# Optimization experiments

Hardware: AMD Instinct MI355X
Metric: run time of the kernel (lower is better)

## Reference

```python
import jax, jax.numpy as jnp
import numpy as np


def setup_inputs() -> dict:
    key = jax.random.key(0)
    k1, k2, k3 = jax.random.split(key, 3)
    worker_num, task_num, edge_type, ability_num = 2048, 2048, 16, 64
    # inputs stacks worker feature rows [:worker_num, :ability_num]
    # and task label-probability rows [worker_num:, :edge_type]
    inputs = jax.random.uniform(k1, (worker_num + task_num, ability_num), dtype=jnp.float32)
    W = jax.random.normal(k2, (ability_num, 1), dtype=jnp.float32)
    b = jax.random.normal(k3, (1,), dtype=jnp.float32)
    return {
        "inputs": inputs,
        "W": W,
        "b": b,
        "worker_num": worker_num,
        "task_num": task_num,
        "edge_type": edge_type,
        "ability_num": ability_num,
    }


def reference(inputs, W, b, worker_num, task_num, edge_type, ability_num):
    # Worker features: [Wn, A]; task label distributions tau: [T, L]
    worker_feature = inputs[:worker_num, :ability_num]
    tau = inputs[worker_num:, :edge_type]
    # prob_part1 = sigmoid(w_i . W + b): per-worker correctness probability, [Wn, 1]
    p1 = jax.nn.sigmoid(worker_feature @ W + b)
    # prob_part2: remaining mass spread over the other (L-1) labels, [Wn, 1]
    p2 = (1.0 - p1) / jnp.float32(edge_type - 1)
    # P[i,j,l] = p1[i]^tau[j,l] * p2[i]^(1 - tau[j,l])  -> [Wn, T, L]
    p1 = p1[:, :, None]  # [Wn, 1, 1]
    p2 = p2[:, :, None]
    tau_b = tau[None, :, :]  # [1, T, L]
    P = jnp.power(p1, tau_b) * jnp.power(p2, 1.0 - tau_b)
    return P
```

## Files before the change

kernel.cpp:

```cpp
#include <hip/hip_runtime.h>

#define WORKERS 2048
#define TASKS   2048
#define ETYPE   16
#define ABIL    64

#define PER_WORKER (TASKS * ETYPE)
#define PER_WORKER4 (PER_WORKER / 4)
#define TOTAL4 (WORKERS * TASKS * ETYPE / 4)

__global__ void prep_kernel(const float* __restrict__ inputs,
                            const float* __restrict__ W,
                            const float* __restrict__ b,
                            float* __restrict__ l1,
                            float* __restrict__ l2,
                            float* __restrict__ tauc) {
    const int tid = blockIdx.x * blockDim.x + threadIdx.x;

    if (tid < WORKERS) {
        const float4* row = reinterpret_cast<const float4*>(inputs + (size_t)tid * ABIL);
        const float4* Wv  = reinterpret_cast<const float4*>(W);
        float acc = 0.0f;
#pragma unroll
        for (int k = 0; k < ABIL / 4; ++k) {
            float4 x = row[k];
            float4 w = Wv[k];
            acc = fmaf(x.x, w.x, acc);
            acc = fmaf(x.y, w.y, acc);
            acc = fmaf(x.z, w.z, acc);
            acc = fmaf(x.w, w.w, acc);
        }
        acc += b[0];
        const float LOG2E = 1.4426950408889634f;
        float e = __builtin_amdgcn_exp2f(-acc * LOG2E);
        float p1 = 1.0f / (1.0f + e);
        float p2 = (1.0f - p1) * (1.0f / (ETYPE - 1));
        l1[tid] = __builtin_amdgcn_logf(p1);
        l2[tid] = __builtin_amdgcn_logf(p2);
    }

    if (tid < PER_WORKER4) {
        int t  = tid >> 2;
        int e0 = (tid & 3) * 4;
        const float4* src = reinterpret_cast<const float4*>(
            inputs + (size_t)(WORKERS + t) * ABIL + e0);
        reinterpret_cast<float4*>(tauc)[tid] = *src;
    }
}

__global__ void __launch_bounds__(256)
pow_kernel(const float* __restrict__ l1,
           const float* __restrict__ l2,
           const float* __restrict__ tauc,
           float4* __restrict__ out) {
    const int stride = gridDim.x * blockDim.x;
    for (int i = blockIdx.x * blockDim.x + threadIdx.x; i < TOTAL4; i += stride) {
        const int w    = i >> 13;
        const int rem4 = i & (PER_WORKER4 - 1);
        const float4 tau = reinterpret_cast<const float4*>(tauc)[rem4];
        const float a = l1[w];
        const float c = l2[w];
        float4 r;
        r.x = __builtin_amdgcn_exp2f(fmaf(tau.x, a, (1.0f - tau.x) * c));
        r.y = __builtin_amdgcn_exp2f(fmaf(tau.y, a, (1.0f - tau.y) * c));
        r.z = __builtin_amdgcn_exp2f(fmaf(tau.z, a, (1.0f - tau.z) * c));
        r.w = __builtin_amdgcn_exp2f(fmaf(tau.w, a, (1.0f - tau.w) * c));
        out[i] = r;
    }
}

extern "C" void kernel_launch(void* const* d_in, const int* in_sizes, int n_in,
                              void* d_out, int out_size, void* d_ws, size_t ws_size,
                              hipStream_t stream) {
    const float* inputs = (const float*)d_in[0];
    const float* W      = (const float*)d_in[1];
    const float* b      = (const float*)d_in[2];

    float* ws   = (float*)d_ws;
    float* l1   = ws;
    float* l2   = ws + WORKERS;
    float* tauc = ws + 2 * WORKERS;

    prep_kernel<<<32, 256, 0, stream>>>(inputs, W, b, l1, l2, tauc);

    const int blocks = 2048;
    pow_kernel<<<blocks, 256, 0, stream>>>(l1, l2, tauc, (float4*)d_out);
}
```

Before: 51.85 us.

## Fuse worker-probability prep into the pow kernel and read tau directly

Removes the separate prep kernel. Each block recomputes its worker's sigmoid dot product and log probabilities, then writes a contiguous half of that worker's output slice, reading tau directly from the strided input rows. This cuts a kernel launch and the workspace write/read, at the cost of redundant per-block dot products and less coalesced tau loads.

```diff
diff --git a/kernel.cpp b/kernel.cpp
--- a/kernel.cpp
+++ b/kernel.cpp
@@ -5,61 +5,48 @@
 #define ETYPE   16
 #define ABIL    64
 
-#define PER_WORKER (TASKS * ETYPE)
-#define PER_WORKER4 (PER_WORKER / 4)
-#define TOTAL4 (WORKERS * TASKS * ETYPE / 4)
-
-__global__ void prep_kernel(const float* __restrict__ inputs,
-                            const float* __restrict__ W,
-                            const float* __restrict__ b,
-                            float* __restrict__ l1,
-                            float* __restrict__ l2,
-                            float* __restrict__ tauc) {
-    const int tid = blockIdx.x * blockDim.x + threadIdx.x;
-
-    if (tid < WORKERS) {
-        const float4* row = reinterpret_cast<const float4*>(inputs + (size_t)tid * ABIL);
-        const float4* Wv  = reinterpret_cast<const float4*>(W);
-        float acc = 0.0f;
-#pragma unroll
-        for (int k = 0; k < ABIL / 4; ++k) {
-            float4 x = row[k];
-            float4 w = Wv[k];
-            acc = fmaf(x.x, w.x, acc);
-            acc = fmaf(x.y, w.y, acc);
-            acc = fmaf(x.z, w.z, acc);
-            acc = fmaf(x.w, w.w, acc);
-        }
-        acc += b[0];
-        const float LOG2E = 1.4426950408889634f;
-        float e = __builtin_amdgcn_exp2f(-acc * LOG2E);
-        float p1 = 1.0f / (1.0f + e);
-        float p2 = (1.0f - p1) * (1.0f / (ETYPE - 1));
-        l1[tid] = __builtin_amdgcn_logf(p1);
-        l2[tid] = __builtin_amdgcn_logf(p2);
-    }
-
-    if (tid < PER_WORKER4) {
-        int t  = tid >> 2;
-        int e0 = (tid & 3) * 4;
-        const float4* src = reinterpret_cast<const float4*>(
-            inputs + (size_t)(WORKERS + t) * ABIL + e0);
-        reinterpret_cast<float4*>(tauc)[tid] = *src;
-    }
-}
+#define F4_PER_WORKER  8192
+#define F4_PER_BLOCK   4096
+#define ITERS          16
 
 __global__ void __launch_bounds__(256)
-pow_kernel(const float* __restrict__ l1,
-           const float* __restrict__ l2,
-           const float* __restrict__ tauc,
-           float4* __restrict__ out) {
-    const int stride = gridDim.x * blockDim.x;
-    for (int i = blockIdx.x * blockDim.x + threadIdx.x; i < TOTAL4; i += stride) {
-        const int w    = i >> 13;
-        const int rem4 = i & (PER_WORKER4 - 1);
-        const float4 tau = reinterpret_cast<const float4*>(tauc)[rem4];
-        const float a = l1[w];
-        const float c = l2[w];
+fused_kernel(const float* __restrict__ inputs,
+             const float* __restrict__ W,
+             const float* __restrict__ b,
+             float4* __restrict__ out) {
+    const int blk  = blockIdx.x;
+    const int w    = blk >> 1;
+    const int half = blk & 1;
+
+    const float4* row = reinterpret_cast<const float4*>(inputs + (size_t)w * ABIL);
+    const float4* Wv  = reinterpret_cast<const float4*>(W);
+    float acc = 0.0f;
+#pragma unroll
+    for (int k = 0; k < ABIL / 4; ++k) {
+        float4 x  = row[k];
+        float4 wv = Wv[k];
+        acc = fmaf(x.x, wv.x, acc);
+        acc = fmaf(x.y, wv.y, acc);
+        acc = fmaf(x.z, wv.z, acc);
+        acc = fmaf(x.w, wv.w, acc);
+    }
+    acc += b[0];
+    const float LOG2E = 1.4426950408889634f;
+    float e  = __builtin_amdgcn_exp2f(-acc * LOG2E);
+    float p1 = 1.0f / (1.0f + e);
+    float p2 = (1.0f - p1) * (1.0f / (ETYPE - 1));
+    const float a = __builtin_amdgcn_logf(p1);
+    const float c = __builtin_amdgcn_logf(p2);
+
+    const int base = w * F4_PER_WORKER + half * F4_PER_BLOCK + (int)threadIdx.x;
+#pragma unroll
+    for (int it = 0; it < ITERS; ++it) {
+        const int i    = base + it * 256;
+        const int rem4 = i & (F4_PER_WORKER - 1);
+        const int t    = rem4 >> 2;
+        const int e0   = (rem4 & 3) * 4;
+        const float4 tau = *reinterpret_cast<const float4*>(
+            inputs + (size_t)(WORKERS + t) * ABIL + e0);
         float4 r;
         r.x = __builtin_amdgcn_exp2f(fmaf(tau.x, a, (1.0f - tau.x) * c));
         r.y = __builtin_amdgcn_exp2f(fmaf(tau.y, a, (1.0f - tau.y) * c));
@@ -76,13 +63,6 @@
     const float* W      = (const float*)d_in[1];
     const float* b      = (const float*)d_in[2];
 
-    float* ws   = (float*)d_ws;
-    float* l1   = ws;
-    float* l2   = ws + WORKERS;
-    float* tauc = ws + 2 * WORKERS;
-
-    prep_kernel<<<32, 256, 0, stream>>>(inputs, W, b, l1, l2, tauc);
-
-    const int blocks = 2048;
-    pow_kernel<<<blocks, 256, 0, stream>>>(l1, l2, tauc, (float4*)d_out);
+    const int blocks = WORKERS * 2;
+    fused_kernel<<<blocks, 256, 0, stream>>>(inputs, W, b, (float4*)d_out);
 }
```

New measurement: 46.22 us, median of 2. 1.12x faster.
